# Kernel optimization log

Hardware: AMD Instinct MI355X
Metric: run time of the kernel (lower is better)

## Reference

```python
import jax, jax.numpy as jnp
import numpy as np

NEG_INF = jnp.float32(-(2.0**32) + 1.0)


def squash(z):
    # z: [B, k_max, out_units]
    sq_norm = jnp.sum(jnp.square(z), axis=-1, keepdims=True)
    scale = sq_norm / (1.0 + sq_norm) / jnp.sqrt(sq_norm + 1e-8)
    return scale * z


def setup_inputs() -> dict:
    key = jax.random.key(0)
    k1, k2, k3, k4 = jax.random.split(key, 4)
    B, L, D_IN, D_OUT, K = 1024, 200, 256, 256, 8
    behavior_embeddings = jax.random.normal(k1, (B, L, D_IN), dtype=jnp.float32)
    seq_len = jax.random.randint(k2, (B, 1), 1, L + 1, dtype=jnp.int32)
    routing_logits = jax.random.normal(k3, (1, K, L), dtype=jnp.float32)  # init_std=1.0
    bilinear_mapping_matrix = jax.random.normal(k4, (D_IN, D_OUT), dtype=jnp.float32)
    return {
        "behavior_embeddings": behavior_embeddings,
        "seq_len": seq_len,
        "routing_logits": routing_logits,
        "bilinear_mapping_matrix": bilinear_mapping_matrix,
    }


def reference(behavior_embeddings, seq_len, routing_logits, bilinear_mapping_matrix):
    ITERATION_TIMES = 3
    B, L, _ = behavior_embeddings.shape
    K = routing_logits.shape[1]

    # mask: [B, 1, L] broadcastable to [B, K, L] (same seq_len for every capsule)
    mask = jnp.arange(L)[None, None, :] < seq_len[:, :, None]

    # bilinear map is loop-invariant: [B, L, out_units]
    mapped = jnp.einsum("ble,eo->blo", behavior_embeddings, bilinear_mapping_matrix)

    logits = routing_logits  # [1, K, L]
    interest_capsules = None
    for _ in range(ITERATION_TIMES):
        logits_pad = jnp.where(mask, jnp.broadcast_to(logits, (B, K, L)), NEG_INF)
        weight = jax.nn.softmax(logits_pad, axis=-1)          # [B, K, L]
        Z = jnp.einsum("bkl,blo->bko", weight, mapped)         # [B, K, out]
        interest_capsules = squash(Z)                          # [B, K, out]
        # delta: sum over batch of capsules @ mapped^T -> [1, K, L]
        delta = jnp.einsum("bko,blo->kl", interest_capsules, mapped)[None]
        logits = logits + delta  # emulates assign_add on non-trainable B

    return interest_capsules.reshape(-1, K, interest_capsules.shape[-1])
```

## Files before the change

kernel.cpp:

```cpp
#include <hip/hip_runtime.h>
#include <cstdint>
#include <cstddef>

#define B_    1024
#define L_    200
#define DIN_  256
#define DOUT_ 256
#define K_    8
#define M_    (B_ * L_)

typedef __attribute__((ext_vector_type(8))) short bf16x8;
typedef __attribute__((ext_vector_type(4))) float f32x4;

__device__ __forceinline__ float bf2f(unsigned short u) {
  union { unsigned int i; float f; } w; w.i = ((unsigned int)u) << 16; return w.f;
}
__device__ __forceinline__ unsigned short f2bf(float f) {
  union { float f; unsigned int i; } w; w.f = f;
  unsigned int x = w.i;
  return (unsigned short)((x + 0x7fffu + ((x >> 16) & 1u)) >> 16);
}

__global__ __launch_bounds__(256)
void wt_prep(const float* __restrict__ W, unsigned short* __restrict__ Wh,
             unsigned short* __restrict__ Wm, unsigned short* __restrict__ Wl)
{
  const int k = blockIdx.x;
  const int n = threadIdx.x;
  float x = W[k * DOUT_ + n];
  unsigned short h = f2bf(x);
  float r = x - bf2f(h);
  unsigned short m = f2bf(r);
  float r2 = r - bf2f(m);
  unsigned short l = f2bf(r2);
  const int k0b = k >> 5, quad = (k >> 3) & 3, j = k & 7;
  const int nt = n >> 4, lr = n & 15;
  const size_t idx = ((((size_t)k0b * 16 + nt) * 64) + (quad * 16 + lr)) * 8 + j;
  Wh[idx] = h;
  Wm[idx] = m;
  Wl[idx] = l;
}

__global__ __launch_bounds__(256, 2)
void gemm_mapped(const float* __restrict__ A,
                 const unsigned short* __restrict__ Wh,
                 const unsigned short* __restrict__ Wm,
                 const unsigned short* __restrict__ Wl,
                 float* __restrict__ C)
{
  const int t    = threadIdx.x;
  const int wave = t >> 6;
  const int lane = t & 63;
  const int quad = lane >> 4;
  const int lr   = lane & 15;
  const int m0   = blockIdx.x * 128 + wave * 32;

  f32x4 acc[2][16];
  #pragma unroll
  for (int mt = 0; mt < 2; ++mt)
    #pragma unroll
    for (int nt = 0; nt < 16; ++nt)
      acc[mt][nt] = (f32x4){0.f, 0.f, 0.f, 0.f};

  bf16x8 Bh[4], Bm[4], Bl[4];
  bf16x8 ah[2], am[2], al[2];
  float4 Af[2][2];

#define BLOAD(K0B, NT, S) do { \
    const size_t _off = (((size_t)(K0B) * 16 + (NT)) * 64 + lane) * 8; \
    Bh[S] = *(const bf16x8*)(Wh + _off); \
    Bm[S] = *(const bf16x8*)(Wm + _off); \
    Bl[S] = *(const bf16x8*)(Wl + _off); \
  } while (0)

  const float* ap0 = A + (size_t)(m0 + lr) * DIN_ + quad * 8;
  const float* ap1 = A + (size_t)(m0 + 16 + lr) * DIN_ + quad * 8;

  Af[0][0] = *(const float4*)(ap0);
  Af[0][1] = *(const float4*)(ap0 + 4);
  Af[1][0] = *(const float4*)(ap1);
  Af[1][1] = *(const float4*)(ap1 + 4);
  BLOAD(0, 0, 0); BLOAD(0, 1, 1); BLOAD(0, 2, 2); BLOAD(0, 3, 3);

  for (int k0b = 0; k0b < 8; ++k0b) {
    #pragma unroll
    for (int mt = 0; mt < 2; ++mt) {
      float xs[8] = {Af[mt][0].x, Af[mt][0].y, Af[mt][0].z, Af[mt][0].w,
                     Af[mt][1].x, Af[mt][1].y, Af[mt][1].z, Af[mt][1].w};
      #pragma unroll
      for (int j = 0; j < 8; ++j) {
        unsigned short h = f2bf(xs[j]);
        float r = xs[j] - bf2f(h);
        unsigned short mm = f2bf(r);
        float r2 = r - bf2f(mm);
        unsigned short ll = f2bf(r2);
        ah[mt][j] = (short)h; am[mt][j] = (short)mm; al[mt][j] = (short)ll;
      }
    }
    if (k0b < 7) {
      const int ko = (k0b + 1) * 32;
      Af[0][0] = *(const float4*)(ap0 + ko);
      Af[0][1] = *(const float4*)(ap0 + ko + 4);
      Af[1][0] = *(const float4*)(ap1 + ko);
      Af[1][1] = *(const float4*)(ap1 + ko + 4);
    }

#define GROUP(NT, S) do { \
    f32x4 c0 = acc[0][NT], c1 = acc[1][NT]; \
    c0 = __builtin_amdgcn_mfma_f32_16x16x32_bf16(ah[0], Bh[S], c0, 0, 0, 0); \
    c1 = __builtin_amdgcn_mfma_f32_16x16x32_bf16(ah[1], Bh[S], c1, 0, 0, 0); \
    c0 = __builtin_amdgcn_mfma_f32_16x16x32_bf16(ah[0], Bm[S], c0, 0, 0, 0); \
    c1 = __builtin_amdgcn_mfma_f32_16x16x32_bf16(ah[1], Bm[S], c1, 0, 0, 0); \
    c0 = __builtin_amdgcn_mfma_f32_16x16x32_bf16(am[0], Bh[S], c0, 0, 0, 0); \
    c1 = __builtin_amdgcn_mfma_f32_16x16x32_bf16(am[1], Bh[S], c1, 0, 0, 0); \
    c0 = __builtin_amdgcn_mfma_f32_16x16x32_bf16(ah[0], Bl[S], c0, 0, 0, 0); \
    c1 = __builtin_amdgcn_mfma_f32_16x16x32_bf16(ah[1], Bl[S], c1, 0, 0, 0); \
    c0 = __builtin_amdgcn_mfma_f32_16x16x32_bf16(am[0], Bm[S], c0, 0, 0, 0); \
    c1 = __builtin_amdgcn_mfma_f32_16x16x32_bf16(am[1], Bm[S], c1, 0, 0, 0); \
    c0 = __builtin_amdgcn_mfma_f32_16x16x32_bf16(al[0], Bh[S], c0, 0, 0, 0); \
    c1 = __builtin_amdgcn_mfma_f32_16x16x32_bf16(al[1], Bh[S], c1, 0, 0, 0); \
    acc[0][NT] = c0; acc[1][NT] = c1; \
  } while (0)

    GROUP(0, 0);  BLOAD(k0b, 4, 0);
    GROUP(1, 1);  BLOAD(k0b, 5, 1);
    GROUP(2, 2);  BLOAD(k0b, 6, 2);
    GROUP(3, 3);  BLOAD(k0b, 7, 3);
    GROUP(4, 0);  BLOAD(k0b, 8, 0);
    GROUP(5, 1);  BLOAD(k0b, 9, 1);
    GROUP(6, 2);  BLOAD(k0b, 10, 2);
    GROUP(7, 3);  BLOAD(k0b, 11, 3);
    GROUP(8, 0);  BLOAD(k0b, 12, 0);
    GROUP(9, 1);  BLOAD(k0b, 13, 1);
    GROUP(10, 2); BLOAD(k0b, 14, 2);
    GROUP(11, 3); BLOAD(k0b, 15, 3);
    GROUP(12, 0);
    GROUP(13, 1);
    GROUP(14, 2);
    GROUP(15, 3);
    if (k0b < 7) {
      BLOAD(k0b + 1, 0, 0); BLOAD(k0b + 1, 1, 1);
      BLOAD(k0b + 1, 2, 2); BLOAD(k0b + 1, 3, 3);
    }
#undef GROUP
  }
#undef BLOAD

  #pragma unroll
  for (int mt = 0; mt < 2; ++mt)
    #pragma unroll
    for (int nt = 0; nt < 16; ++nt)
      #pragma unroll
      for (int r = 0; r < 4; ++r) {
        int row = m0 + mt * 16 + quad * 4 + r;
        C[(size_t)row * DOUT_ + nt * 16 + lr] = acc[mt][nt][r];
      }
}

__global__ __launch_bounds__(256)
void z_kernel(const float* __restrict__ mapped, const float* __restrict__ logits,
              const int* __restrict__ seq_len, float* __restrict__ caps)
{
  const int b    = blockIdx.x;
  const int t    = threadIdx.x;
  const int lane = t & 63;
  const int wave = t >> 6;
  const int len  = seq_len[b];
  __shared__ float w[K_][204];
  __shared__ float red[4][K_][DOUT_];

  #pragma unroll
  for (int kk = 0; kk < 2; ++kk) {
    const int k = wave * 2 + kk;
    float v[4];
    float mx = -3.4028235e38f;
    #pragma unroll
    for (int i = 0; i < 4; ++i) {
      int l = lane + 64 * i;
      v[i] = (l < len) ? logits[k * L_ + l] : -3.4028235e38f;
      mx = fmaxf(mx, v[i]);
    }
    #pragma unroll
    for (int s = 1; s < 64; s <<= 1) mx = fmaxf(mx, __shfl_xor(mx, s, 64));
    float e[4]; float sum = 0.f;
    #pragma unroll
    for (int i = 0; i < 4; ++i) {
      int l = lane + 64 * i;
      e[i] = (l < len) ? __expf(v[i] - mx) : 0.f;
      sum += e[i];
    }
    #pragma unroll
    for (int s = 1; s < 64; s <<= 1) sum += __shfl_xor(sum, s, 64);
    float inv = 1.f / sum;
    #pragma unroll
    for (int i = 0; i < 4; ++i) {
      int l = lane + 64 * i;
      if (l < 204) w[k][l] = e[i] * inv;
    }
  }
  __syncthreads();

  f32x4 acc[K_];
  #pragma unroll
  for (int k = 0; k < K_; ++k) acc[k] = (f32x4){0.f, 0.f, 0.f, 0.f};
  const float* mp = mapped + (size_t)b * L_ * DOUT_ + lane * 4;
  const int lceil = (len + 3) & ~3;
  for (int l = wave * 4; l < lceil; l += 16) {
    float4 m0 = *(const float4*)(mp + (size_t)(l + 0) * DOUT_);
    float4 m1 = *(const float4*)(mp + (size_t)(l + 1) * DOUT_);
    float4 m2 = *(const float4*)(mp + (size_t)(l + 2) * DOUT_);
    float4 m3 = *(const float4*)(mp + (size_t)(l + 3) * DOUT_);
    #pragma unroll
    for (int k = 0; k < K_; ++k) {
      float4 wv = *(const float4*)&w[k][l];
      f32x4 c = acc[k];
      c.x += wv.x * m0.x + wv.y * m1.x + wv.z * m2.x + wv.w * m3.x;
      c.y += wv.x * m0.y + wv.y * m1.y + wv.z * m2.y + wv.w * m3.y;
      c.z += wv.x * m0.z + wv.y * m1.z + wv.z * m2.z + wv.w * m3.z;
      c.w += wv.x * m0.w + wv.y * m1.w + wv.z * m2.w + wv.w * m3.w;
      acc[k] = c;
    }
  }
  #pragma unroll
  for (int k = 0; k < K_; ++k)
    *(f32x4*)&red[wave][k][lane * 4] = acc[k];
  __syncthreads();

  #pragma unroll
  for (int kk = 0; kk < 2; ++kk) {
    const int k = wave * 2 + kk;
    float4 s0 = *(const float4*)&red[0][k][lane * 4];
    float4 s1 = *(const float4*)&red[1][k][lane * 4];
    float4 s2 = *(const float4*)&red[2][k][lane * 4];
    float4 s3 = *(const float4*)&red[3][k][lane * 4];
    float4 z;
    z.x = (s0.x + s1.x) + (s2.x + s3.x);
    z.y = (s0.y + s1.y) + (s2.y + s3.y);
    z.z = (s0.z + s1.z) + (s2.z + s3.z);
    z.w = (s0.w + s1.w) + (s2.w + s3.w);
    float sq = z.x * z.x + z.y * z.y + z.z * z.z + z.w * z.w;
    #pragma unroll
    for (int s = 1; s < 64; s <<= 1) sq += __shfl_xor(sq, s, 64);
    float scale = sq / ((1.f + sq) * sqrtf(sq + 1e-8f));
    float4 o;
    o.x = scale * z.x; o.y = scale * z.y; o.z = scale * z.z; o.w = scale * z.w;
    *(float4*)&caps[((size_t)b * K_ + k) * DOUT_ + lane * 4] = o;
  }
}

__global__ __launch_bounds__(256)
void delta_kernel(const float* __restrict__ mapped, const float* __restrict__ caps,
                  float* __restrict__ partials)
{
  const int t    = threadIdx.x;
  const int lane = t & 63;
  const int wave = t >> 6;
  const int lc   = blockIdx.x % 13;
  const int bc   = blockIdx.x / 13;
  const int bsub = (wave >> 1) * 8;
  const int lsub = (wave & 1) * 8;
  const int l0   = lc * 16 + lsub;
  const int b0   = bc * 16 + bsub;
  const int o4   = lane * 4;

  float acc[K_][8];
  #pragma unroll
  for (int k = 0; k < K_; ++k)
    #pragma unroll
    for (int ll = 0; ll < 8; ++ll) acc[k][ll] = 0.f;

  for (int bi = 0; bi < 8; ++bi) {
    const int b = b0 + bi;
    const float* cp = caps + (size_t)b * (K_ * DOUT_) + o4;
    const float* mp = mapped + ((size_t)b * L_ + l0) * DOUT_ + o4;
    float4 cv[K_], mv[8];
    #pragma unroll
    for (int k = 0; k < K_; ++k) cv[k] = *(const float4*)(cp + (size_t)k * DOUT_);
    #pragma unroll
    for (int ll = 0; ll < 8; ++ll) {
      mv[ll] = (l0 + ll < L_) ? *(const float4*)(mp + (size_t)ll * DOUT_)
                              : make_float4(0.f, 0.f, 0.f, 0.f);
    }
    #pragma unroll
    for (int k = 0; k < K_; ++k)
      #pragma unroll
      for (int ll = 0; ll < 8; ++ll)
        acc[k][ll] += cv[k].x * mv[ll].x + cv[k].y * mv[ll].y
                    + cv[k].z * mv[ll].z + cv[k].w * mv[ll].w;
  }

  float out = 0.f;
  #pragma unroll
  for (int k = 0; k < K_; ++k)
    #pragma unroll
    for (int ll = 0; ll < 8; ++ll) {
      float v = acc[k][ll];
      v += __shfl_xor(v, 1, 64);
      v += __shfl_xor(v, 2, 64);
      v += __shfl_xor(v, 4, 64);
      v += __shfl_xor(v, 8, 64);
      v += __shfl_xor(v, 16, 64);
      v += __shfl_xor(v, 32, 64);
      if (lane == k * 8 + ll) out = v;
    }
  __shared__ float red[4][64];
  red[wave][lane] = out;
  __syncthreads();
  if (wave < 2) {
    float v = red[wave][lane] + red[wave + 2][lane];
    const int k  = lane >> 3;
    const int ll = lane & 7;
    const int gl = lc * 16 + wave * 8 + ll;
    if (gl < L_) partials[((size_t)bc * K_ + k) * L_ + gl] = v;
  }
}

__global__ __launch_bounds__(256)
void init_logits(const float* __restrict__ rlog, float* __restrict__ logits)
{
  int i = blockIdx.x * 256 + threadIdx.x;
  if (i < K_ * L_) logits[i] = rlog[i];
}

__global__ __launch_bounds__(256)
void reduce_kernel(const float* __restrict__ partials, float* __restrict__ logits)
{
  int i = blockIdx.x * 256 + threadIdx.x;
  if (i < K_ * L_) {
    float s = 0.f;
    #pragma unroll 4
    for (int bc = 0; bc < 64; ++bc) s += partials[bc * (K_ * L_) + i];
    logits[i] += s;
  }
}

extern "C" void kernel_launch(void* const* d_in, const int* in_sizes, int n_in,
                              void* d_out, int out_size, void* d_ws, size_t ws_size,
                              hipStream_t stream)
{
  const float* behav = (const float*)d_in[0];
  const int*   slen  = (const int*)d_in[1];
  const float* rlog  = (const float*)d_in[2];
  const float* W     = (const float*)d_in[3];
  float* caps = (float*)d_out;

  char* ws = (char*)d_ws;
  float* logitsW  = (float*)ws;
  float* partials = (float*)(ws + 8192);
  unsigned short* Wh = (unsigned short*)(ws + 458752);
  unsigned short* Wm = (unsigned short*)(ws + 589824);
  unsigned short* Wl = (unsigned short*)(ws + 720896);
  float* mapped   = (float*)(ws + (1 << 20));

  init_logits<<<dim3(7), 256, 0, stream>>>(rlog, logitsW);
  wt_prep<<<dim3(256), 256, 0, stream>>>(W, Wh, Wm, Wl);
  gemm_mapped<<<dim3(1600), 256, 0, stream>>>(behav, Wh, Wm, Wl, mapped);
  for (int it = 0; it < 3; ++it) {
    z_kernel<<<dim3(B_), 256, 0, stream>>>(mapped, logitsW, slen, caps);
    if (it < 2) {
      delta_kernel<<<dim3(13 * 64), 256, 0, stream>>>(mapped, caps, partials);
      reduce_kernel<<<dim3(7), 256, 0, stream>>>(partials, logitsW);
    }
  }
}
```

Measured before the change: 645.3 us.

## Stage GEMM operands in shared memory and map one batch per wave in z_kernel

The GEMM kernel now cooperatively loads each K-slice of the three bf16 weight splits and a 128x32 fp32 activation tile into LDS, guarded by barriers. Previously every wave streamed the weights from global memory into registers with software prefetch. The intent is to cut redundant global weight traffic and register pressure, at the cost of losing the load/compute overlap and adding two syncs per K-step. Separately, z_kernel assigns one batch row per wave instead of one per block, which removes the cross-wave LDS reduction and barriers. In exchange, each wave walks the full sequence serially.

Result: slower. 729.0 us (+13.0%).

```diff
diff --git a/kernel.cpp b/kernel.cpp
--- a/kernel.cpp
+++ b/kernel.cpp
@@ -41,6 +41,8 @@
   Wl[idx] = l;
 }
 
+#define APAD 36
+
 __global__ __launch_bounds__(256, 2)
 void gemm_mapped(const float* __restrict__ A,
                  const unsigned short* __restrict__ Wh,
@@ -53,7 +55,11 @@
   const int lane = t & 63;
   const int quad = lane >> 4;
   const int lr   = lane & 15;
-  const int m0   = blockIdx.x * 128 + wave * 32;
+  const int blk0 = blockIdx.x * 128;
+  const int m0   = blk0 + wave * 32;
+
+  __shared__ unsigned short Bs[3 * 16 * 64 * 8];
+  __shared__ float As[128][APAD];
 
   f32x4 acc[2][16];
   #pragma unroll
@@ -62,31 +68,39 @@
     for (int nt = 0; nt < 16; ++nt)
       acc[mt][nt] = (f32x4){0.f, 0.f, 0.f, 0.f};
 
-  bf16x8 Bh[4], Bm[4], Bl[4];
   bf16x8 ah[2], am[2], al[2];
-  float4 Af[2][2];
-
-#define BLOAD(K0B, NT, S) do { \
-    const size_t _off = (((size_t)(K0B) * 16 + (NT)) * 64 + lane) * 8; \
-    Bh[S] = *(const bf16x8*)(Wh + _off); \
-    Bm[S] = *(const bf16x8*)(Wm + _off); \
-    Bl[S] = *(const bf16x8*)(Wl + _off); \
-  } while (0)
-
-  const float* ap0 = A + (size_t)(m0 + lr) * DIN_ + quad * 8;
-  const float* ap1 = A + (size_t)(m0 + 16 + lr) * DIN_ + quad * 8;
-
-  Af[0][0] = *(const float4*)(ap0);
-  Af[0][1] = *(const float4*)(ap0 + 4);
-  Af[1][0] = *(const float4*)(ap1);
-  Af[1][1] = *(const float4*)(ap1 + 4);
-  BLOAD(0, 0, 0); BLOAD(0, 1, 1); BLOAD(0, 2, 2); BLOAD(0, 3, 3);
+
+  const uint4* WhU = (const uint4*)Wh;
+  const uint4* WmU = (const uint4*)Wm;
+  const uint4* WlU = (const uint4*)Wl;
+  uint4* BsU = (uint4*)Bs;
+
+  const int arow = t >> 1;
+  const int acol = (t & 1) * 16;
+  const float* abase = A + (size_t)(blk0 + arow) * DIN_ + acol;
 
   for (int k0b = 0; k0b < 8; ++k0b) {
     #pragma unroll
+    for (int i = 0; i < 4; ++i) {
+      const int idx = t + i * 256;
+      BsU[idx]        = WhU[k0b * 1024 + idx];
+      BsU[1024 + idx] = WmU[k0b * 1024 + idx];
+      BsU[2048 + idx] = WlU[k0b * 1024 + idx];
+    }
+    {
+      const float* ap = abase + k0b * 32;
+      #pragma unroll
+      for (int i = 0; i < 4; ++i)
+        *(float4*)&As[arow][acol + i * 4] = *(const float4*)(ap + i * 4);
+    }
+    __syncthreads();
+
+    #pragma unroll
     for (int mt = 0; mt < 2; ++mt) {
-      float xs[8] = {Af[mt][0].x, Af[mt][0].y, Af[mt][0].z, Af[mt][0].w,
-                     Af[mt][1].x, Af[mt][1].y, Af[mt][1].z, Af[mt][1].w};
+      const int row = wave * 32 + mt * 16 + lr;
+      float4 f0 = *(const float4*)&As[row][quad * 8];
+      float4 f1 = *(const float4*)&As[row][quad * 8 + 4];
+      float xs[8] = {f0.x, f0.y, f0.z, f0.w, f1.x, f1.y, f1.z, f1.w};
       #pragma unroll
       for (int j = 0; j < 8; ++j) {
         unsigned short h = f2bf(xs[j]);
@@ -97,54 +111,29 @@
         ah[mt][j] = (short)h; am[mt][j] = (short)mm; al[mt][j] = (short)ll;
       }
     }
-    if (k0b < 7) {
-      const int ko = (k0b + 1) * 32;
-      Af[0][0] = *(const float4*)(ap0 + ko);
-      Af[0][1] = *(const float4*)(ap0 + ko + 4);
-      Af[1][0] = *(const float4*)(ap1 + ko);
-      Af[1][1] = *(const float4*)(ap1 + ko + 4);
-    }
-
-#define GROUP(NT, S) do { \
-    f32x4 c0 = acc[0][NT], c1 = acc[1][NT]; \
-    c0 = __builtin_amdgcn_mfma_f32_16x16x32_bf16(ah[0], Bh[S], c0, 0, 0, 0); \
-    c1 = __builtin_amdgcn_mfma_f32_16x16x32_bf16(ah[1], Bh[S], c1, 0, 0, 0); \
-    c0 = __builtin_amdgcn_mfma_f32_16x16x32_bf16(ah[0], Bm[S], c0, 0, 0, 0); \
-    c1 = __builtin_amdgcn_mfma_f32_16x16x32_bf16(ah[1], Bm[S], c1, 0, 0, 0); \
-    c0 = __builtin_amdgcn_mfma_f32_16x16x32_bf16(am[0], Bh[S], c0, 0, 0, 0); \
-    c1 = __builtin_amdgcn_mfma_f32_16x16x32_bf16(am[1], Bh[S], c1, 0, 0, 0); \
-    c0 = __builtin_amdgcn_mfma_f32_16x16x32_bf16(ah[0], Bl[S], c0, 0, 0, 0); \
-    c1 = __builtin_amdgcn_mfma_f32_16x16x32_bf16(ah[1], Bl[S], c1, 0, 0, 0); \
-    c0 = __builtin_amdgcn_mfma_f32_16x16x32_bf16(am[0], Bm[S], c0, 0, 0, 0); \
-    c1 = __builtin_amdgcn_mfma_f32_16x16x32_bf16(am[1], Bm[S], c1, 0, 0, 0); \
-    c0 = __builtin_amdgcn_mfma_f32_16x16x32_bf16(al[0], Bh[S], c0, 0, 0, 0); \
-    c1 = __builtin_amdgcn_mfma_f32_16x16x32_bf16(al[1], Bh[S], c1, 0, 0, 0); \
-    acc[0][NT] = c0; acc[1][NT] = c1; \
-  } while (0)
-
-    GROUP(0, 0);  BLOAD(k0b, 4, 0);
-    GROUP(1, 1);  BLOAD(k0b, 5, 1);
-    GROUP(2, 2);  BLOAD(k0b, 6, 2);
-    GROUP(3, 3);  BLOAD(k0b, 7, 3);
-    GROUP(4, 0);  BLOAD(k0b, 8, 0);
-    GROUP(5, 1);  BLOAD(k0b, 9, 1);
-    GROUP(6, 2);  BLOAD(k0b, 10, 2);
-    GROUP(7, 3);  BLOAD(k0b, 11, 3);
-    GROUP(8, 0);  BLOAD(k0b, 12, 0);
-    GROUP(9, 1);  BLOAD(k0b, 13, 1);
-    GROUP(10, 2); BLOAD(k0b, 14, 2);
-    GROUP(11, 3); BLOAD(k0b, 15, 3);
-    GROUP(12, 0);
-    GROUP(13, 1);
-    GROUP(14, 2);
-    GROUP(15, 3);
-    if (k0b < 7) {
-      BLOAD(k0b + 1, 0, 0); BLOAD(k0b + 1, 1, 1);
-      BLOAD(k0b + 1, 2, 2); BLOAD(k0b + 1, 3, 3);
-    }
-#undef GROUP
-  }
-#undef BLOAD
+
+    #pragma unroll
+    for (int nt = 0; nt < 16; ++nt) {
+      bf16x8 bh = *(const bf16x8*)&Bs[(0 * 16 + nt) * 512 + lane * 8];
+      bf16x8 bm = *(const bf16x8*)&Bs[(1 * 16 + nt) * 512 + lane * 8];
+      bf16x8 bl = *(const bf16x8*)&Bs[(2 * 16 + nt) * 512 + lane * 8];
+      f32x4 c0 = acc[0][nt], c1 = acc[1][nt];
+      c0 = __builtin_amdgcn_mfma_f32_16x16x32_bf16(ah[0], bh, c0, 0, 0, 0);
+      c1 = __builtin_amdgcn_mfma_f32_16x16x32_bf16(ah[1], bh, c1, 0, 0, 0);
+      c0 = __builtin_amdgcn_mfma_f32_16x16x32_bf16(ah[0], bm, c0, 0, 0, 0);
+      c1 = __builtin_amdgcn_mfma_f32_16x16x32_bf16(ah[1], bm, c1, 0, 0, 0);
+      c0 = __builtin_amdgcn_mfma_f32_16x16x32_bf16(am[0], bh, c0, 0, 0, 0);
+      c1 = __builtin_amdgcn_mfma_f32_16x16x32_bf16(am[1], bh, c1, 0, 0, 0);
+      c0 = __builtin_amdgcn_mfma_f32_16x16x32_bf16(ah[0], bl, c0, 0, 0, 0);
+      c1 = __builtin_amdgcn_mfma_f32_16x16x32_bf16(ah[1], bl, c1, 0, 0, 0);
+      c0 = __builtin_amdgcn_mfma_f32_16x16x32_bf16(am[0], bm, c0, 0, 0, 0);
+      c1 = __builtin_amdgcn_mfma_f32_16x16x32_bf16(am[1], bm, c1, 0, 0, 0);
+      c0 = __builtin_amdgcn_mfma_f32_16x16x32_bf16(al[0], bh, c0, 0, 0, 0);
+      c1 = __builtin_amdgcn_mfma_f32_16x16x32_bf16(al[1], bh, c1, 0, 0, 0);
+      acc[0][nt] = c0; acc[1][nt] = c1;
+    }
+    __syncthreads();
+  }
 
   #pragma unroll
   for (int mt = 0; mt < 2; ++mt)
@@ -161,17 +150,15 @@
 void z_kernel(const float* __restrict__ mapped, const float* __restrict__ logits,
               const int* __restrict__ seq_len, float* __restrict__ caps)
 {
-  const int b    = blockIdx.x;
   const int t    = threadIdx.x;
   const int lane = t & 63;
   const int wave = t >> 6;
+  const int b    = blockIdx.x * 4 + wave;
   const int len  = seq_len[b];
-  __shared__ float w[K_][204];
-  __shared__ float red[4][K_][DOUT_];
-
-  #pragma unroll
-  for (int kk = 0; kk < 2; ++kk) {
-    const int k = wave * 2 + kk;
+  __shared__ float w[4][K_][204];
+
+  #pragma unroll
+  for (int k = 0; k < K_; ++k) {
     float v[4];
     float mx = -3.4028235e38f;
     #pragma unroll
@@ -195,24 +182,23 @@
     #pragma unroll
     for (int i = 0; i < 4; ++i) {
       int l = lane + 64 * i;
-      if (l < 204) w[k][l] = e[i] * inv;
-    }
-  }
-  __syncthreads();
+      if (l < 204) w[wave][k][l] = e[i] * inv;
+    }
+  }
 
   f32x4 acc[K_];
   #pragma unroll
   for (int k = 0; k < K_; ++k) acc[k] = (f32x4){0.f, 0.f, 0.f, 0.f};
   const float* mp = mapped + (size_t)b * L_ * DOUT_ + lane * 4;
   const int lceil = (len + 3) & ~3;
-  for (int l = wave * 4; l < lceil; l += 16) {
+  for (int l = 0; l < lceil; l += 4) {
     float4 m0 = *(const float4*)(mp + (size_t)(l + 0) * DOUT_);
     float4 m1 = *(const float4*)(mp + (size_t)(l + 1) * DOUT_);
     float4 m2 = *(const float4*)(mp + (size_t)(l + 2) * DOUT_);
     float4 m3 = *(const float4*)(mp + (size_t)(l + 3) * DOUT_);
     #pragma unroll
     for (int k = 0; k < K_; ++k) {
-      float4 wv = *(const float4*)&w[k][l];
+      float4 wv = *(const float4*)&w[wave][k][l];
       f32x4 c = acc[k];
       c.x += wv.x * m0.x + wv.y * m1.x + wv.z * m2.x + wv.w * m3.x;
       c.y += wv.x * m0.y + wv.y * m1.y + wv.z * m2.y + wv.w * m3.y;
@@ -221,29 +207,17 @@
       acc[k] = c;
     }
   }
-  #pragma unroll
-  for (int k = 0; k < K_; ++k)
-    *(f32x4*)&red[wave][k][lane * 4] = acc[k];
-  __syncthreads();
-
-  #pragma unroll
-  for (int kk = 0; kk < 2; ++kk) {
-    const int k = wave * 2 + kk;
-    float4 s0 = *(const float4*)&red[0][k][lane * 4];
-    float4 s1 = *(const float4*)&red[1][k][lane * 4];
-    float4 s2 = *(const float4*)&red[2][k][lane * 4];
-    float4 s3 = *(const float4*)&red[3][k][lane * 4];
-    float4 z;
-    z.x = (s0.x + s1.x) + (s2.x + s3.x);
-    z.y = (s0.y + s1.y) + (s2.y + s3.y);
-    z.z = (s0.z + s1.z) + (s2.z + s3.z);
-    z.w = (s0.w + s1.w) + (s2.w + s3.w);
-    float sq = z.x * z.x + z.y * z.y + z.z * z.z + z.w * z.w;
+
+  #pragma unroll
+  for (int k = 0; k < K_; ++k) {
+    float sq = acc[k].x * acc[k].x + acc[k].y * acc[k].y
+             + acc[k].z * acc[k].z + acc[k].w * acc[k].w;
     #pragma unroll
     for (int s = 1; s < 64; s <<= 1) sq += __shfl_xor(sq, s, 64);
     float scale = sq / ((1.f + sq) * sqrtf(sq + 1e-8f));
     float4 o;
-    o.x = scale * z.x; o.y = scale * z.y; o.z = scale * z.z; o.w = scale * z.w;
+    o.x = scale * acc[k].x; o.y = scale * acc[k].y;
+    o.z = scale * acc[k].z; o.w = scale * acc[k].w;
     *(float4*)&caps[((size_t)b * K_ + k) * DOUT_ + lane * 4] = o;
   }
 }
@@ -356,7 +330,7 @@
   wt_prep<<<dim3(256), 256, 0, stream>>>(W, Wh, Wm, Wl);
   gemm_mapped<<<dim3(1600), 256, 0, stream>>>(behav, Wh, Wm, Wl, mapped);
   for (int it = 0; it < 3; ++it) {
-    z_kernel<<<dim3(B_), 256, 0, stream>>>(mapped, logitsW, slen, caps);
+    z_kernel<<<dim3(B_ / 4), 256, 0, stream>>>(mapped, logitsW, slen, caps);
     if (it < 2) {
       delta_kernel<<<dim3(13 * 64), 256, 0, stream>>>(mapped, caps, partials);
       reduce_kernel<<<dim3(7), 256, 0, stream>>>(partials, logitsW);
```
